# Performance work log

Hardware: AMD Instinct MI355X
Metric: run time of the kernel (lower is better)

The kernel has to match this reference:

```python
import jax, jax.numpy as jnp
import numpy as np

B, S, D = 4, 2048, 1024
H, DQ, DV = 16, 64, 64
LN_EPS = 1e-3  # keras LayerNormalization default


def _layer_norm(x, gamma, beta):
    mu = jnp.mean(x, axis=-1, keepdims=True)
    var = jnp.mean(jnp.square(x - mu), axis=-1, keepdims=True)
    return (x - mu) * jax.lax.rsqrt(var + LN_EPS) * gamma + beta


def setup_inputs() -> dict:
    key = jax.random.key(0)
    ks = jax.random.split(key, 6)
    x = jax.random.normal(ks[0], (B, S, D), jnp.float32)
    lengths = jax.random.randint(ks[1], (B,), 1, S + 1).astype(jnp.int32)
    scale = 0.02
    return {
        "query_sequences": x,
        "key_value_sequences": x,  # identical -> self-attention branch
        "key_value_sequence_lengths": lengths,
        "W_q": jax.random.normal(ks[2], (D, H * DQ), jnp.float32) * scale,
        "b_q": jnp.zeros((H * DQ,), jnp.float32),
        "W_kv": jax.random.normal(ks[3], (D, H * (DQ + DV)), jnp.float32) * scale,
        "b_kv": jnp.zeros((H * (DQ + DV),), jnp.float32),
        "W_o": jax.random.normal(ks[4], (H * DV, D), jnp.float32) * scale,
        "b_o": jnp.zeros((D,), jnp.float32),
        "ln_gamma": jnp.ones((D,), jnp.float32),
        "ln_beta": jnp.zeros((D,), jnp.float32),
    }


def reference(query_sequences, key_value_sequences, key_value_sequence_lengths,
              W_q, b_q, W_kv, b_kv, W_o, b_o, ln_gamma, ln_beta):
    # data-dependent self-attention detection, as in the TF code
    self_att = jnp.all(query_sequences == key_value_sequences)

    q_norm = _layer_norm(query_sequences, ln_gamma, ln_beta)
    kv_used = jnp.where(self_att, _layer_norm(key_value_sequences, ln_gamma, ln_beta),
                        key_value_sequences)
    residual = q_norm

    Q = (q_norm @ W_q + b_q).reshape(B, S, H, DQ)          # b q h d
    KV = kv_used @ W_kv + b_kv
    K = KV[..., : H * DQ].reshape(B, S, H, DQ)              # b k h d
    V = KV[..., H * DQ :].reshape(B, S, H, DV)              # b k h d

    scores = jnp.einsum("bqhd,bkhd->bhqk", Q, K) / np.sqrt(DQ).astype(np.float32)

    # key padding mask: key position < true length
    not_pad = (jnp.arange(S, dtype=jnp.int32)[None, None, None, :]
               < key_value_sequence_lengths[:, None, None, None])
    scores = jnp.where(not_pad, scores, -jnp.inf)
    # in_decoder=False -> no causal mask branch

    attn = jax.nn.softmax(scores, axis=-1)                  # dropout is identity at inference
    ctx = jnp.einsum("bhqk,bkhd->bqhd", attn, V).reshape(B, S, H * DV)
    out = ctx @ W_o + b_o + residual
    return out
```

## Files before the change

kernel.cpp:

```cpp
#include <hip/hip_runtime.h>
#include <hip/hip_bf16.h>
#include <cstdint>
#include <cmath>


#define DEV static __device__ __forceinline__

typedef float  f32x4 __attribute__((ext_vector_type(4)));
typedef short  s16x8 __attribute__((ext_vector_type(8)));
typedef short  s16x4 __attribute__((ext_vector_type(4)));
typedef __bf16 bf16x8 __attribute__((ext_vector_type(8)));
typedef unsigned int u32x4 __attribute__((ext_vector_type(4)));

DEV void gload_lds16(const void* g, void* l) {
  __builtin_amdgcn_global_load_lds(
      (const __attribute__((address_space(1))) unsigned int*)g,
      (__attribute__((address_space(3))) unsigned int*)l, 16, 0, 0);
}

DEV bf16x8 ldsv(const void* p) {
  return __builtin_bit_cast(bf16x8, *(const s16x8*)p);
}

DEV f32x4 mfma16(bf16x8 a, bf16x8 b, f32x4 c) {
  return __builtin_amdgcn_mfma_f32_16x16x32_bf16(a, b, c, 0, 0, 0);
}

DEV unsigned short f2b(float f) {
  __hip_bfloat16 h = __float2bfloat16(f);
  return __builtin_bit_cast(unsigned short, h);
}

DEV unsigned int cvt_pk_bf16(float lo, float hi) {
  unsigned int r;
  asm("v_cvt_pk_bf16_f32 %0, %1, %2" : "=v"(r) : "v"(lo), "v"(hi));
  return r;
}

__global__ __launch_bounds__(256) void ln_kernel(
    const float* __restrict__ x, const float* __restrict__ gamma,
    const float* __restrict__ beta, __hip_bfloat16* __restrict__ out)
{
  const int row = blockIdx.x, t = threadIdx.x;
  const float4 v = ((const float4*)(x + (size_t)row * 1024))[t];
  float s = v.x + v.y + v.z + v.w;
  float q = v.x * v.x + v.y * v.y + v.z * v.z + v.w * v.w;
#pragma unroll
  for (int m = 1; m < 64; m <<= 1) { s += __shfl_xor(s, m, 64); q += __shfl_xor(q, m, 64); }
  __shared__ float red[8];
  if ((t & 63) == 0) { red[t >> 6] = s; red[4 + (t >> 6)] = q; }
  __syncthreads();
  s = red[0] + red[1] + red[2] + red[3];
  q = red[4] + red[5] + red[6] + red[7];
  const float mu = s * (1.f / 1024.f);
  const float var = q * (1.f / 1024.f) - mu * mu;
  const float rs = rsqrtf(var + 1e-3f);
  const float4 g = ((const float4*)gamma)[t];
  const float4 bt = ((const float4*)beta)[t];
  s16x4 o;
  o[0] = (short)f2b((v.x - mu) * rs * g.x + bt.x);
  o[1] = (short)f2b((v.y - mu) * rs * g.y + bt.y);
  o[2] = (short)f2b((v.z - mu) * rs * g.z + bt.z);
  o[3] = (short)f2b((v.w - mu) * rs * g.w + bt.w);
  *(s16x4*)((short*)out + (size_t)row * 1024 + t * 4) = o;
}

__global__ __launch_bounds__(256) void wconv(
    const float* __restrict__ W, int N, __hip_bfloat16* __restrict__ Wt)
{
  __shared__ float tile[64][65];
  const int t = threadIdx.x;
  const int k0 = blockIdx.x * 64, n0 = blockIdx.y * 64;
#pragma unroll
  for (int p = 0; p < 4; ++p) {
    int r = p * 16 + (t >> 4), c4 = (t & 15) * 4;
    float4 v = *(const float4*)(W + (size_t)(k0 + r) * N + n0 + c4);
    tile[r][c4] = v.x; tile[r][c4 + 1] = v.y; tile[r][c4 + 2] = v.z; tile[r][c4 + 3] = v.w;
  }
  __syncthreads();
#pragma unroll
  for (int p = 0; p < 4; ++p) {
    int n = p * 16 + (t >> 4), kc = (t & 15) * 4;
    s16x4 o;
    o[0] = (short)f2b(tile[kc][n]);     o[1] = (short)f2b(tile[kc + 1][n]);
    o[2] = (short)f2b(tile[kc + 2][n]); o[3] = (short)f2b(tile[kc + 3][n]);
    *(s16x4*)((short*)Wt + (size_t)(n0 + n) * 1024 + k0 + kc) = o;
  }
}

template<bool RESID>
__global__ __launch_bounds__(256, 2) void gemm_bt(
    const __hip_bfloat16* __restrict__ A, const __hip_bfloat16* __restrict__ Bt,
    const float* __restrict__ bias0, const float* __restrict__ bias1, int split,
    const __hip_bfloat16* __restrict__ resid,
    __hip_bfloat16* __restrict__ outb, float* __restrict__ outf, int Ncols)
{
  __shared__ __align__(16) short sA[128 * 64];
  __shared__ __align__(16) short sB[128 * 64];
  const int t = threadIdx.x, l = t & 63, w = t >> 6;
  const int wr = w >> 1, wc = w & 1, lr = l & 15, lg = l >> 4;
  const int row0 = blockIdx.y * 128, col0 = blockIdx.x * 128;
  f32x4 acc[4][4] = {};

  for (int kt = 0; kt < 1024; kt += 64) {
#pragma unroll
    for (int p = 0; p < 4; ++p) {
      const int L = p * 4096 + t * 16;
      const int r = L >> 7, c = ((L >> 4) & 7) ^ (r & 7);
      gload_lds16((const char*)A + ((size_t)(row0 + r) * 1024 + kt + c * 8) * 2, (char*)sA + L);
    }
#pragma unroll
    for (int p = 0; p < 4; ++p) {
      const int L = p * 4096 + t * 16;
      const int r = L >> 7, c = ((L >> 4) & 7) ^ (r & 7);
      gload_lds16((const char*)Bt + ((size_t)(col0 + r) * 1024 + kt + c * 8) * 2, (char*)sB + L);
    }
    __syncthreads();

    bf16x8 af[4][2], bfr[4][2];
#pragma unroll
    for (int mb = 0; mb < 4; ++mb) {
      const int ar = wr * 64 + mb * 16 + lr;
#pragma unroll
      for (int kk = 0; kk < 2; ++kk)
        af[mb][kk] = ldsv((const char*)sA + ar * 128 + (((kk * 4 + lg) ^ (ar & 7)) * 16));
    }
#pragma unroll
    for (int nb = 0; nb < 4; ++nb) {
      const int br = wc * 64 + nb * 16 + lr;
#pragma unroll
      for (int kk = 0; kk < 2; ++kk)
        bfr[nb][kk] = ldsv((const char*)sB + br * 128 + (((kk * 4 + lg) ^ (br & 7)) * 16));
    }
#pragma unroll
    for (int kk = 0; kk < 2; ++kk)
#pragma unroll
      for (int mb = 0; mb < 4; ++mb)
#pragma unroll
        for (int nb = 0; nb < 4; ++nb)
          acc[mb][nb] = mfma16(af[mb][kk], bfr[nb][kk], acc[mb][nb]);
    __syncthreads();
  }

#pragma unroll
  for (int mb = 0; mb < 4; ++mb) {
    const int rbase = row0 + wr * 64 + mb * 16 + lg * 4;
#pragma unroll
    for (int nb = 0; nb < 4; ++nb) {
      const int col = col0 + wc * 64 + nb * 16 + lr;
      const float bias = (col < split) ? bias0[col] : bias1[col - split];
#pragma unroll
      for (int jr = 0; jr < 4; ++jr) {
        const size_t idx = (size_t)(rbase + jr) * Ncols + col;
        float v = acc[mb][nb][jr] + bias;
        if (RESID) outf[idx] = v + __bfloat162float(resid[idx]);
        else       outb[idx] = __float2bfloat16(v);
      }
    }
  }
}

__global__ __launch_bounds__(256) void vtrans(
    const __hip_bfloat16* __restrict__ qkv, __hip_bfloat16* __restrict__ vt)
{
  __shared__ __align__(16) short tile[64][72];
  const int t = threadIdx.x;
  const int s0 = blockIdx.x * 64;
  const int bh = blockIdx.y, b = bh >> 4, h = bh & 15;
#pragma unroll
  for (int p = 0; p < 2; ++p) {
    int idx = p * 256 + t;
    int r = idx >> 3, c = idx & 7;
    s16x8 vv = *(const s16x8*)((const short*)qkv +
        (size_t)(b * 2048 + s0 + r) * 3072 + 2048 + h * 64 + c * 8);
    *(s16x8*)((char*)tile + r * 144 + c * 16) = vv;
  }
  __syncthreads();
  const int dv = t >> 2, sc = (t & 3) * 16;
  s16x8 a, bvec;
#pragma unroll
  for (int e = 0; e < 8; ++e) a[e] = tile[sc + e][dv];
#pragma unroll
  for (int e = 0; e < 8; ++e) bvec[e] = tile[sc + 8 + e][dv];
  short* dst = (short*)vt + (size_t)(bh * 64 + dv) * 2048 + s0 + sc;
  *(s16x8*)dst = a;
  *(s16x8*)(dst + 8) = bvec;
}

__global__ __launch_bounds__(256, 4) void attn_kernel(
    const __hip_bfloat16* __restrict__ qkv, const __hip_bfloat16* __restrict__ vt,
    const int* __restrict__ lens, __hip_bfloat16* __restrict__ ctx)
{
  __shared__ __align__(16) short sK[2][64 * 64];
  __shared__ __align__(16) short sV[2][64 * 64];
  const int t = threadIdx.x, l = t & 63, w = t >> 6;
  const int lr = l & 15, lg = l >> 4;
  const int bh = blockIdx.y, b = bh >> 4, h = bh & 15;
  const int q0 = blockIdx.x * 128 + w * 32;
  const int len = lens[b];
  const float NEG = -__builtin_inff();
  const float QSC = 0.18033688f;

  bf16x8 qf[2][2];
#pragma unroll
  for (int mbt = 0; mbt < 2; ++mbt)
#pragma unroll
    for (int kk = 0; kk < 2; ++kk) {
      bf16x8 r = ldsv((const char*)qkv +
          ((size_t)(b * 2048 + q0 + mbt * 16 + lr) * 3072 + h * 64 + kk * 32 + lg * 8) * 2);
#pragma unroll
      for (int e = 0; e < 8; ++e) qf[mbt][kk][e] = (__bf16)((float)r[e] * QSC);
    }

  f32x4 o[4][2] = {};
  float mrun[2] = {NEG, NEG}, ssum[2] = {0.f, 0.f};

  auto stage = [&](short* dK, short* dV, int kv0) {
#pragma unroll
    for (int p = 0; p < 2; ++p) {
      const int L = p * 4096 + t * 16;
      const int r = L >> 7, c = ((L >> 4) & 7) ^ (r & 7);
      gload_lds16((const char*)qkv +
          ((size_t)(b * 2048 + kv0 + r) * 3072 + 1024 + h * 64 + c * 8) * 2, (char*)dK + L);
    }
#pragma unroll
    for (int p = 0; p < 2; ++p) {
      const int L = p * 4096 + t * 16;
      const int r = L >> 7, c = ((L >> 4) & 7) ^ (r & 7);
      gload_lds16((const char*)vt +
          ((size_t)(bh * 64 + r) * 2048 + kv0 + c * 8) * 2, (char*)dV + L);
    }
  };

  const int nt = (len + 63) >> 6;
  short* curK = sK[0]; short* nxtK = sK[1];
  short* curV = sV[0]; short* nxtV = sV[1];
  stage(curK, curV, 0);

  const int srcA = (lg & 1) * 32 + lr;
  const int srcB = srcA + 16;

  for (int ti = 0; ti < nt; ++ti) {
    const int kv0 = ti * 64;
    if (ti + 1 < nt) {
      stage(nxtK, nxtV, kv0 + 64);
      asm volatile("s_waitcnt vmcnt(4)" ::: "memory");
    } else {
      asm volatile("s_waitcnt vmcnt(0)" ::: "memory");
    }
    __builtin_amdgcn_s_barrier();
    asm volatile("" ::: "memory");

    f32x4 sf[2][4] = {};
    __builtin_amdgcn_s_setprio(1);
#pragma unroll
    for (int kk = 0; kk < 2; ++kk) {
      bf16x8 ak[4];
#pragma unroll
      for (int nbt = 0; nbt < 4; ++nbt) {
        const int br = nbt * 16 + lr;
        ak[nbt] = ldsv((const char*)curK + br * 128 + (((kk * 4 + lg) ^ (br & 7)) * 16));
      }
#pragma unroll
      for (int mbt = 0; mbt < 2; ++mbt)
#pragma unroll
        for (int nbt = 0; nbt < 4; ++nbt)
          sf[mbt][nbt] = mfma16(ak[nbt], qf[mbt][kk], sf[mbt][nbt]);
    }
    __builtin_amdgcn_s_setprio(0);

    if (kv0 + 64 > len) {
#pragma unroll
      for (int nbt = 0; nbt < 4; ++nbt)
#pragma unroll
        for (int jr = 0; jr < 4; ++jr)
          if (kv0 + nbt * 16 + lg * 4 + jr >= len) {
            sf[0][nbt][jr] = NEG;
            sf[1][nbt][jr] = NEG;
          }
    }

    float rm[2];
#pragma unroll
    for (int mbt = 0; mbt < 2; ++mbt) {
      f32x4 m4 = sf[mbt][0];
      m4 = __builtin_elementwise_max(m4, sf[mbt][1]);
      m4 = __builtin_elementwise_max(m4, sf[mbt][2]);
      m4 = __builtin_elementwise_max(m4, sf[mbt][3]);
      float m0 = fmaxf(fmaxf(m4[0], m4[1]), fmaxf(m4[2], m4[3]));
      m0 = fmaxf(m0, __shfl_xor(m0, 16, 64));
      m0 = fmaxf(m0, __shfl_xor(m0, 32, 64));
      rm[mbt] = m0;
    }
    const bool need = (rm[0] > mrun[0] + 3.f) || (rm[1] > mrun[1] + 3.f);
    if (__any(need)) {
#pragma unroll
      for (int mbt = 0; mbt < 2; ++mbt) {
        const float mnew = fmaxf(mrun[mbt], rm[mbt]);
        const float corr = __builtin_amdgcn_exp2f(mrun[mbt] - mnew);
        mrun[mbt] = mnew;
        ssum[mbt] *= corr;
#pragma unroll
        for (int nbt2 = 0; nbt2 < 4; ++nbt2) o[nbt2][mbt] *= corr;
      }
    }
    unsigned int W0[2][4], W1[2][4];
#pragma unroll
    for (int mbt = 0; mbt < 2; ++mbt) {
      f32x4 ts = {0.f, 0.f, 0.f, 0.f};
#pragma unroll
      for (int nbt = 0; nbt < 4; ++nbt) {
        f32x4 pe;
#pragma unroll
        for (int jr = 0; jr < 4; ++jr)
          pe[jr] = __builtin_amdgcn_exp2f(sf[mbt][nbt][jr] - mrun[mbt]);
        ts += pe;
        W0[mbt][nbt] = cvt_pk_bf16(pe[0], pe[1]);
        W1[mbt][nbt] = cvt_pk_bf16(pe[2], pe[3]);
      }
      ssum[mbt] += (ts[0] + ts[1]) + (ts[2] + ts[3]);
    }

#pragma unroll
    for (int c = 0; c < 2; ++c) {
      bf16x8 vf[4], pb[2];
#pragma unroll
      for (int nbt2 = 0; nbt2 < 4; ++nbt2) {
        const int vr = nbt2 * 16 + lr;
        vf[nbt2] = ldsv((const char*)curV + vr * 128 + (((c * 4 + lg) ^ (vr & 7)) * 16));
      }
#pragma unroll
      for (int mbt = 0; mbt < 2; ++mbt) {
        const unsigned int selW0 = (lg & 2) ? W0[mbt][2 * c + 1] : W0[mbt][2 * c];
        const unsigned int selW1 = (lg & 2) ? W1[mbt][2 * c + 1] : W1[mbt][2 * c];
        u32x4 bw;
        bw[0] = __shfl((int)selW0, srcA, 64);
        bw[1] = __shfl((int)selW1, srcA, 64);
        bw[2] = __shfl((int)selW0, srcB, 64);
        bw[3] = __shfl((int)selW1, srcB, 64);
        pb[mbt] = __builtin_bit_cast(bf16x8, bw);
      }
      __builtin_amdgcn_s_setprio(1);
#pragma unroll
      for (int nbt2 = 0; nbt2 < 4; ++nbt2)
#pragma unroll
        for (int mbt = 0; mbt < 2; ++mbt)
          o[nbt2][mbt] = mfma16(vf[nbt2], pb[mbt], o[nbt2][mbt]);
      __builtin_amdgcn_s_setprio(0);
    }

    asm volatile("s_waitcnt lgkmcnt(0)" ::: "memory");
    __builtin_amdgcn_s_barrier();
    asm volatile("" ::: "memory");
    short* tk = curK; curK = nxtK; nxtK = tk;
    short* tv = curV; curV = nxtV; nxtV = tv;
  }

  float inv[2];
#pragma unroll
  for (int mbt = 0; mbt < 2; ++mbt) {
    float s = ssum[mbt];
    s += __shfl_xor(s, 16, 64);
    s += __shfl_xor(s, 32, 64);
    inv[mbt] = 1.f / s;
  }
  char* eb = (char*)sK + w * 4352;
#pragma unroll
  for (int mbt = 0; mbt < 2; ++mbt)
#pragma unroll
    for (int nbt2 = 0; nbt2 < 4; ++nbt2)
#pragma unroll
      for (int jr = 0; jr < 4; ++jr)
        *(short*)(eb + (mbt * 16 + lr) * 136 + (nbt2 * 16 + lg * 4 + jr) * 2) =
            (short)f2b(o[nbt2][mbt][jr] * inv[mbt]);
  asm volatile("s_waitcnt lgkmcnt(0)" ::: "memory");
  __builtin_amdgcn_sched_barrier(0);
  const int qi = l >> 1, half = l & 1;
#pragma unroll
  for (int i = 0; i < 4; ++i) {
    s16x8 v = *(const s16x8*)(eb + qi * 136 + half * 64 + i * 16);
    *(s16x8*)((short*)ctx + (size_t)(b * 2048 + q0 + qi) * 1024 + h * 64 + half * 32 + i * 8) = v;
  }
}

extern "C" void kernel_launch(void* const* d_in, const int* in_sizes, int n_in,
                              void* d_out, int out_size, void* d_ws, size_t ws_size,
                              hipStream_t stream)
{
  const float* x     = (const float*)d_in[0];
  const int*   lens  = (const int*)d_in[2];
  const float* Wq    = (const float*)d_in[3];
  const float* bq    = (const float*)d_in[4];
  const float* Wkv   = (const float*)d_in[5];
  const float* bkv   = (const float*)d_in[6];
  const float* Wo    = (const float*)d_in[7];
  const float* bo    = (const float*)d_in[8];
  const float* gamma = (const float*)d_in[9];
  const float* beta  = (const float*)d_in[10];
  float* out = (float*)d_out;

  char* ws = (char*)d_ws;
  __hip_bfloat16* ln  = (__hip_bfloat16*)(ws);
  __hip_bfloat16* qkv = (__hip_bfloat16*)(ws + ((size_t)16 << 20));
  __hip_bfloat16* vt  = (__hip_bfloat16*)(ws + ((size_t)64 << 20));
  __hip_bfloat16* ctx = (__hip_bfloat16*)(ws + ((size_t)80 << 20));
  __hip_bfloat16* wt  = (__hip_bfloat16*)(ws + ((size_t)96 << 20));
  __hip_bfloat16* wot = (__hip_bfloat16*)(ws + ((size_t)102 << 20));

  ln_kernel<<<dim3(8192), dim3(256), 0, stream>>>(x, gamma, beta, ln);
  wconv<<<dim3(16, 16), dim3(256), 0, stream>>>(Wq, 1024, wt);
  wconv<<<dim3(16, 32), dim3(256), 0, stream>>>(Wkv, 2048, wt + (size_t)1024 * 1024);
  wconv<<<dim3(16, 16), dim3(256), 0, stream>>>(Wo, 1024, wot);
  gemm_bt<false><<<dim3(24, 64), dim3(256), 0, stream>>>(
      ln, wt, bq, bkv, 1024, (const __hip_bfloat16*)nullptr,
      qkv, (float*)nullptr, 3072);
  vtrans<<<dim3(32, 64), dim3(256), 0, stream>>>(qkv, vt);
  attn_kernel<<<dim3(16, 64), dim3(256), 0, stream>>>(qkv, vt, lens, ctx);
  gemm_bt<true><<<dim3(8, 64), dim3(256), 0, stream>>>(
      ctx, wot, bo, bo, 1 << 30, ln,
      (__hip_bfloat16*)nullptr, out, 1024);
}
```

Measured before the change: 174.9 us.

## Add 256x256 triple-buffered QKV GEMM and restructure attention to 16-row waves

Replaces the QKV projection GEMM with a new 512-thread kernel that uses 256x256 tiles, a three-stage LDS ring fed by direct global-to-LDS loads, interleaved barriers and an XCD-aware block remap. The attention kernel now gives each wave 16 query rows instead of 32, doubling the grid, with a swizzled block order. It also reads V fragments straight from global memory instead of staging them in LDS. The output GEMM loses its template and split-bias logic. These changes aim to raise GEMM data reuse and attention occupancy, at the cost of more K reloads per query and uncoalesced global V reads.

```diff
diff --git a/kernel.cpp b/kernel.cpp
--- a/kernel.cpp
+++ b/kernel.cpp
@@ -36,6 +36,8 @@
   asm("v_cvt_pk_bf16_f32 %0, %1, %2" : "=v"(r) : "v"(lo), "v"(hi));
   return r;
 }
+
+#define MEMFENCE asm volatile("" ::: "memory")
 
 __global__ __launch_bounds__(256) void ln_kernel(
     const float* __restrict__ x, const float* __restrict__ gamma,
@@ -88,12 +90,113 @@
   }
 }
 
-template<bool RESID>
+__global__ __launch_bounds__(512, 2) void gemm8(
+    const __hip_bfloat16* __restrict__ A, const __hip_bfloat16* __restrict__ Bt,
+    const float* __restrict__ bias0, const float* __restrict__ bias1, int split,
+    __hip_bfloat16* __restrict__ outb)
+{
+  __shared__ __align__(16) short sA[3 * 8192];
+  __shared__ __align__(16) short sB[3 * 8192];
+  const int t = threadIdx.x, l = t & 63, w = t >> 6;
+  const int wr = w >> 2, wc = w & 3, lr = l & 15, lg = l >> 4;
+  int bid = blockIdx.x;
+  const int cpx = gridDim.x >> 3;
+  bid = (bid & 7) * cpx + (bid >> 3);
+  const int bx = bid % 12, by = bid / 12;
+  const int row0 = by * 256, col0 = bx * 256;
+
+  f32x4 acc[8][4] = {};
+  const int NT = 32;
+
+  auto stageA = [&](int buf, int kt) {
+#pragma unroll
+    for (int p = 0; p < 2; ++p) {
+      const int L = p * 8192 + t * 16;
+      const int r = L >> 6, c = (L >> 4) & 3;
+      const int j = c ^ (r & 3);
+      gload_lds16((const char*)A + ((size_t)(row0 + r) * 1024 + kt + j * 8) * 2,
+                  (char*)sA + buf * 16384 + L);
+    }
+  };
+  auto stageB = [&](int buf, int kt) {
+#pragma unroll
+    for (int p = 0; p < 2; ++p) {
+      const int L = p * 8192 + t * 16;
+      const int r = L >> 6, c = (L >> 4) & 3;
+      const int j = c ^ (r & 3);
+      gload_lds16((const char*)Bt + ((size_t)(col0 + r) * 1024 + kt + j * 8) * 2,
+                  (char*)sB + buf * 16384 + L);
+    }
+  };
+
+  stageA(0, 0);  stageB(0, 0);
+  stageA(1, 32); stageB(1, 32);
+  asm volatile("s_waitcnt vmcnt(4)" ::: "memory");
+  MEMFENCE; __builtin_amdgcn_s_barrier(); MEMFENCE;
+
+#pragma unroll 1
+  for (int ti = 0; ti < NT; ++ti) {
+    const int cur = ti % 3, nx2 = (ti + 2) % 3;
+    const char* bA = (const char*)sA + cur * 16384;
+    const char* bB = (const char*)sB + cur * 16384;
+    bf16x8 bfr[4], af[4];
+#pragma unroll
+    for (int nb = 0; nb < 4; ++nb) {
+      const int br = wc * 64 + nb * 16 + lr;
+      bfr[nb] = ldsv(bB + br * 64 + ((lg ^ (br & 3)) * 16));
+    }
+#pragma unroll
+    for (int mb = 0; mb < 4; ++mb) {
+      const int ar = wr * 128 + mb * 16 + lr;
+      af[mb] = ldsv(bA + ar * 64 + ((lg ^ (ar & 3)) * 16));
+    }
+    if (ti + 2 < NT) stageA(nx2, (ti + 2) * 32);
+    MEMFENCE; __builtin_amdgcn_s_barrier(); MEMFENCE;
+    __builtin_amdgcn_s_setprio(1);
+#pragma unroll
+    for (int mb = 0; mb < 4; ++mb)
+#pragma unroll
+      for (int nb = 0; nb < 4; ++nb)
+        acc[mb][nb] = mfma16(af[mb], bfr[nb], acc[mb][nb]);
+    __builtin_amdgcn_s_setprio(0);
+    MEMFENCE; __builtin_amdgcn_s_barrier(); MEMFENCE;
+#pragma unroll
+    for (int mb = 0; mb < 4; ++mb) {
+      const int ar = wr * 128 + 64 + mb * 16 + lr;
+      af[mb] = ldsv(bA + ar * 64 + ((lg ^ (ar & 3)) * 16));
+    }
+    if (ti + 2 < NT) stageB(nx2, (ti + 2) * 32);
+    MEMFENCE; __builtin_amdgcn_s_barrier(); MEMFENCE;
+    __builtin_amdgcn_s_setprio(1);
+#pragma unroll
+    for (int mb = 0; mb < 4; ++mb)
+#pragma unroll
+      for (int nb = 0; nb < 4; ++nb)
+        acc[mb + 4][nb] = mfma16(af[mb], bfr[nb], acc[mb + 4][nb]);
+    __builtin_amdgcn_s_setprio(0);
+    if (ti + 2 < NT) asm volatile("s_waitcnt vmcnt(4)" ::: "memory");
+    else             asm volatile("s_waitcnt vmcnt(0)" ::: "memory");
+    MEMFENCE; __builtin_amdgcn_s_barrier(); MEMFENCE;
+  }
+
+#pragma unroll
+  for (int mb = 0; mb < 8; ++mb) {
+    const int rbase = row0 + wr * 128 + mb * 16 + lg * 4;
+#pragma unroll
+    for (int nb = 0; nb < 4; ++nb) {
+      const int col = col0 + wc * 64 + nb * 16 + lr;
+      const float bias = (col < split) ? bias0[col] : bias1[col - split];
+#pragma unroll
+      for (int jr = 0; jr < 4; ++jr)
+        outb[(size_t)(rbase + jr) * 3072 + col] = __float2bfloat16(acc[mb][nb][jr] + bias);
+    }
+  }
+}
+
 __global__ __launch_bounds__(256, 2) void gemm_bt(
     const __hip_bfloat16* __restrict__ A, const __hip_bfloat16* __restrict__ Bt,
-    const float* __restrict__ bias0, const float* __restrict__ bias1, int split,
-    const __hip_bfloat16* __restrict__ resid,
-    __hip_bfloat16* __restrict__ outb, float* __restrict__ outf, int Ncols)
+    const float* __restrict__ bias0,
+    const __hip_bfloat16* __restrict__ resid, float* __restrict__ outf)
 {
   __shared__ __align__(16) short sA[128 * 64];
   __shared__ __align__(16) short sB[128 * 64];
@@ -148,13 +251,11 @@
 #pragma unroll
     for (int nb = 0; nb < 4; ++nb) {
       const int col = col0 + wc * 64 + nb * 16 + lr;
-      const float bias = (col < split) ? bias0[col] : bias1[col - split];
+      const float bias = bias0[col];
 #pragma unroll
       for (int jr = 0; jr < 4; ++jr) {
-        const size_t idx = (size_t)(rbase + jr) * Ncols + col;
-        float v = acc[mb][nb][jr] + bias;
-        if (RESID) outf[idx] = v + __bfloat162float(resid[idx]);
-        else       outb[idx] = __float2bfloat16(v);
+        const size_t idx = (size_t)(rbase + jr) * 1024 + col;
+        outf[idx] = acc[mb][nb][jr] + bias + __bfloat162float(resid[idx]);
       }
     }
   }
@@ -192,30 +293,29 @@
     const int* __restrict__ lens, __hip_bfloat16* __restrict__ ctx)
 {
   __shared__ __align__(16) short sK[2][64 * 64];
-  __shared__ __align__(16) short sV[2][64 * 64];
   const int t = threadIdx.x, l = t & 63, w = t >> 6;
   const int lr = l & 15, lg = l >> 4;
-  const int bh = blockIdx.y, b = bh >> 4, h = bh & 15;
-  const int q0 = blockIdx.x * 128 + w * 32;
+  int bid = blockIdx.x;
+  bid = (bid & 7) * 256 + (bid >> 3);
+  const int qb = bid & 31, bh = bid >> 5, b = bh >> 4, h = bh & 15;
+  const int q0w = qb * 64 + w * 16;
   const int len = lens[b];
   const float NEG = -__builtin_inff();
   const float QSC = 0.18033688f;
 
-  bf16x8 qf[2][2];
-#pragma unroll
-  for (int mbt = 0; mbt < 2; ++mbt)
-#pragma unroll
-    for (int kk = 0; kk < 2; ++kk) {
-      bf16x8 r = ldsv((const char*)qkv +
-          ((size_t)(b * 2048 + q0 + mbt * 16 + lr) * 3072 + h * 64 + kk * 32 + lg * 8) * 2);
-#pragma unroll
-      for (int e = 0; e < 8; ++e) qf[mbt][kk][e] = (__bf16)((float)r[e] * QSC);
-    }
-
-  f32x4 o[4][2] = {};
-  float mrun[2] = {NEG, NEG}, ssum[2] = {0.f, 0.f};
-
-  auto stage = [&](short* dK, short* dV, int kv0) {
+  bf16x8 qf[2];
+#pragma unroll
+  for (int kk = 0; kk < 2; ++kk) {
+    bf16x8 r = ldsv((const char*)qkv +
+        ((size_t)(b * 2048 + q0w + lr) * 3072 + h * 64 + kk * 32 + lg * 8) * 2);
+#pragma unroll
+    for (int e = 0; e < 8; ++e) qf[kk][e] = (__bf16)((float)r[e] * QSC);
+  }
+
+  f32x4 o[4] = {};
+  float mrun = NEG, ssum = 0.f;
+
+  auto stageK = [&](short* dK, int kv0) {
 #pragma unroll
     for (int p = 0; p < 2; ++p) {
       const int L = p * 4096 + t * 16;
@@ -223,19 +323,11 @@
       gload_lds16((const char*)qkv +
           ((size_t)(b * 2048 + kv0 + r) * 3072 + 1024 + h * 64 + c * 8) * 2, (char*)dK + L);
     }
-#pragma unroll
-    for (int p = 0; p < 2; ++p) {
-      const int L = p * 4096 + t * 16;
-      const int r = L >> 7, c = ((L >> 4) & 7) ^ (r & 7);
-      gload_lds16((const char*)vt +
-          ((size_t)(bh * 64 + r) * 2048 + kv0 + c * 8) * 2, (char*)dV + L);
-    }
   };
 
   const int nt = (len + 63) >> 6;
   short* curK = sK[0]; short* nxtK = sK[1];
-  short* curV = sV[0]; short* nxtV = sV[1];
-  stage(curK, curV, 0);
+  stageK(curK, 0);
 
   const int srcA = (lg & 1) * 32 + lr;
   const int srcB = srcA + 16;
@@ -243,15 +335,22 @@
   for (int ti = 0; ti < nt; ++ti) {
     const int kv0 = ti * 64;
     if (ti + 1 < nt) {
-      stage(nxtK, nxtV, kv0 + 64);
-      asm volatile("s_waitcnt vmcnt(4)" ::: "memory");
+      stageK(nxtK, kv0 + 64);
+      asm volatile("s_waitcnt vmcnt(2)" ::: "memory");
     } else {
       asm volatile("s_waitcnt vmcnt(0)" ::: "memory");
     }
-    __builtin_amdgcn_s_barrier();
-    asm volatile("" ::: "memory");
-
-    f32x4 sf[2][4] = {};
+    MEMFENCE; __builtin_amdgcn_s_barrier(); MEMFENCE;
+
+    bf16x8 vf[4][2];
+#pragma unroll
+    for (int nbt2 = 0; nbt2 < 4; ++nbt2)
+#pragma unroll
+      for (int c = 0; c < 2; ++c)
+        vf[nbt2][c] = ldsv((const char*)vt +
+            ((size_t)(bh * 64 + nbt2 * 16 + lr) * 2048 + kv0 + (c * 4 + lg) * 8) * 2);
+
+    f32x4 sf[4] = {};
     __builtin_amdgcn_s_setprio(1);
 #pragma unroll
     for (int kk = 0; kk < 2; ++kk) {
@@ -262,10 +361,8 @@
         ak[nbt] = ldsv((const char*)curK + br * 128 + (((kk * 4 + lg) ^ (br & 7)) * 16));
       }
 #pragma unroll
-      for (int mbt = 0; mbt < 2; ++mbt)
-#pragma unroll
-        for (int nbt = 0; nbt < 4; ++nbt)
-          sf[mbt][nbt] = mfma16(ak[nbt], qf[mbt][kk], sf[mbt][nbt]);
+      for (int nbt = 0; nbt < 4; ++nbt)
+        sf[nbt] = mfma16(ak[nbt], qf[kk], sf[nbt]);
     }
     __builtin_amdgcn_s_setprio(0);
 
@@ -274,112 +371,81 @@
       for (int nbt = 0; nbt < 4; ++nbt)
 #pragma unroll
         for (int jr = 0; jr < 4; ++jr)
-          if (kv0 + nbt * 16 + lg * 4 + jr >= len) {
-            sf[0][nbt][jr] = NEG;
-            sf[1][nbt][jr] = NEG;
-          }
-    }
-
-    float rm[2];
-#pragma unroll
-    for (int mbt = 0; mbt < 2; ++mbt) {
-      f32x4 m4 = sf[mbt][0];
-      m4 = __builtin_elementwise_max(m4, sf[mbt][1]);
-      m4 = __builtin_elementwise_max(m4, sf[mbt][2]);
-      m4 = __builtin_elementwise_max(m4, sf[mbt][3]);
-      float m0 = fmaxf(fmaxf(m4[0], m4[1]), fmaxf(m4[2], m4[3]));
-      m0 = fmaxf(m0, __shfl_xor(m0, 16, 64));
-      m0 = fmaxf(m0, __shfl_xor(m0, 32, 64));
-      rm[mbt] = m0;
-    }
-    const bool need = (rm[0] > mrun[0] + 3.f) || (rm[1] > mrun[1] + 3.f);
-    if (__any(need)) {
-#pragma unroll
-      for (int mbt = 0; mbt < 2; ++mbt) {
-        const float mnew = fmaxf(mrun[mbt], rm[mbt]);
-        const float corr = __builtin_amdgcn_exp2f(mrun[mbt] - mnew);
-        mrun[mbt] = mnew;
-        ssum[mbt] *= corr;
-#pragma unroll
-        for (int nbt2 = 0; nbt2 < 4; ++nbt2) o[nbt2][mbt] *= corr;
-      }
-    }
-    unsigned int W0[2][4], W1[2][4];
-#pragma unroll
-    for (int mbt = 0; mbt < 2; ++mbt) {
+          if (kv0 + nbt * 16 + lg * 4 + jr >= len) sf[nbt][jr] = NEG;
+    }
+
+    f32x4 m4 = sf[0];
+    m4 = __builtin_elementwise_max(m4, sf[1]);
+    m4 = __builtin_elementwise_max(m4, sf[2]);
+    m4 = __builtin_elementwise_max(m4, sf[3]);
+    float rm = fmaxf(fmaxf(m4[0], m4[1]), fmaxf(m4[2], m4[3]));
+    rm = fmaxf(rm, __shfl_xor(rm, 16, 64));
+    rm = fmaxf(rm, __shfl_xor(rm, 32, 64));
+    if (__any(rm > mrun + 3.f)) {
+      const float mnew = fmaxf(mrun, rm);
+      const float corr = __builtin_amdgcn_exp2f(mrun - mnew);
+      mrun = mnew;
+      ssum *= corr;
+#pragma unroll
+      for (int nbt2 = 0; nbt2 < 4; ++nbt2) o[nbt2] *= corr;
+    }
+    unsigned int W0[4], W1[4];
+    {
       f32x4 ts = {0.f, 0.f, 0.f, 0.f};
 #pragma unroll
       for (int nbt = 0; nbt < 4; ++nbt) {
         f32x4 pe;
 #pragma unroll
         for (int jr = 0; jr < 4; ++jr)
-          pe[jr] = __builtin_amdgcn_exp2f(sf[mbt][nbt][jr] - mrun[mbt]);
+          pe[jr] = __builtin_amdgcn_exp2f(sf[nbt][jr] - mrun);
         ts += pe;
-        W0[mbt][nbt] = cvt_pk_bf16(pe[0], pe[1]);
-        W1[mbt][nbt] = cvt_pk_bf16(pe[2], pe[3]);
+        W0[nbt] = cvt_pk_bf16(pe[0], pe[1]);
+        W1[nbt] = cvt_pk_bf16(pe[2], pe[3]);
       }
-      ssum[mbt] += (ts[0] + ts[1]) + (ts[2] + ts[3]);
+      ssum += (ts[0] + ts[1]) + (ts[2] + ts[3]);
     }
 
 #pragma unroll
     for (int c = 0; c < 2; ++c) {
-      bf16x8 vf[4], pb[2];
-#pragma unroll
-      for (int nbt2 = 0; nbt2 < 4; ++nbt2) {
-        const int vr = nbt2 * 16 + lr;
-        vf[nbt2] = ldsv((const char*)curV + vr * 128 + (((c * 4 + lg) ^ (vr & 7)) * 16));
-      }
-#pragma unroll
-      for (int mbt = 0; mbt < 2; ++mbt) {
-        const unsigned int selW0 = (lg & 2) ? W0[mbt][2 * c + 1] : W0[mbt][2 * c];
-        const unsigned int selW1 = (lg & 2) ? W1[mbt][2 * c + 1] : W1[mbt][2 * c];
-        u32x4 bw;
-        bw[0] = __shfl((int)selW0, srcA, 64);
-        bw[1] = __shfl((int)selW1, srcA, 64);
-        bw[2] = __shfl((int)selW0, srcB, 64);
-        bw[3] = __shfl((int)selW1, srcB, 64);
-        pb[mbt] = __builtin_bit_cast(bf16x8, bw);
-      }
+      const unsigned int selW0 = (lg & 2) ? W0[2 * c + 1] : W0[2 * c];
+      const unsigned int selW1 = (lg & 2) ? W1[2 * c + 1] : W1[2 * c];
+      u32x4 bw;
+      bw[0] = __shfl((int)selW0, srcA, 64);
+      bw[1] = __shfl((int)selW1, srcA, 64);
+      bw[2] = __shfl((int)selW0, srcB, 64);
+      bw[3] = __shfl((int)selW1, srcB, 64);
+      const bf16x8 pb = __builtin_bit_cast(bf16x8, bw);
       __builtin_amdgcn_s_setprio(1);
 #pragma unroll
       for (int nbt2 = 0; nbt2 < 4; ++nbt2)
-#pragma unroll
-        for (int mbt = 0; mbt < 2; ++mbt)
-          o[nbt2][mbt] = mfma16(vf[nbt2], pb[mbt], o[nbt2][mbt]);
+        o[nbt2] = mfma16(vf[nbt2][c], pb, o[nbt2]);
       __builtin_amdgcn_s_setprio(0);
     }
 
     asm volatile("s_waitcnt lgkmcnt(0)" ::: "memory");
-    __builtin_amdgcn_s_barrier();
-    asm volatile("" ::: "memory");
+    MEMFENCE; __builtin_amdgcn_s_barrier(); MEMFENCE;
     short* tk = curK; curK = nxtK; nxtK = tk;
-    short* tv = curV; curV = nxtV; nxtV = tv;
-  }
-
-  float inv[2];
-#pragma unroll
-  for (int mbt = 0; mbt < 2; ++mbt) {
-    float s = ssum[mbt];
-    s += __shfl_xor(s, 16, 64);
-    s += __shfl_xor(s, 32, 64);
-    inv[mbt] = 1.f / s;
-  }
-  char* eb = (char*)sK + w * 4352;
-#pragma unroll
-  for (int mbt = 0; mbt < 2; ++mbt)
-#pragma unroll
-    for (int nbt2 = 0; nbt2 < 4; ++nbt2)
-#pragma unroll
-      for (int jr = 0; jr < 4; ++jr)
-        *(short*)(eb + (mbt * 16 + lr) * 136 + (nbt2 * 16 + lg * 4 + jr) * 2) =
-            (short)f2b(o[nbt2][mbt][jr] * inv[mbt]);
+  }
+
+  float s = ssum;
+  s += __shfl_xor(s, 16, 64);
+  s += __shfl_xor(s, 32, 64);
+  const float inv = 1.f / s;
+  char* eb = (char*)sK + w * 2176;
+#pragma unroll
+  for (int nbt2 = 0; nbt2 < 4; ++nbt2)
+#pragma unroll
+    for (int jr = 0; jr < 4; ++jr)
+      *(short*)(eb + lr * 136 + (nbt2 * 16 + lg * 4 + jr) * 2) =
+          (short)f2b(o[nbt2][jr] * inv);
   asm volatile("s_waitcnt lgkmcnt(0)" ::: "memory");
   __builtin_amdgcn_sched_barrier(0);
-  const int qi = l >> 1, half = l & 1;
-#pragma unroll
-  for (int i = 0; i < 4; ++i) {
-    s16x8 v = *(const s16x8*)(eb + qi * 136 + half * 64 + i * 16);
-    *(s16x8*)((short*)ctx + (size_t)(b * 2048 + q0 + qi) * 1024 + h * 64 + half * 32 + i * 8) = v;
+  const int qi = l >> 2, pt = l & 3;
+#pragma unroll
+  for (int i = 0; i < 2; ++i) {
+    const int ch = pt * 2 + i;
+    s16x8 v = *(const s16x8*)(eb + qi * 136 + ch * 16);
+    *(s16x8*)((short*)ctx + (size_t)(b * 2048 + q0w + qi) * 1024 + h * 64 + ch * 8) = v;
   }
 }
 
@@ -411,12 +477,8 @@
   wconv<<<dim3(16, 16), dim3(256), 0, stream>>>(Wq, 1024, wt);
   wconv<<<dim3(16, 32), dim3(256), 0, stream>>>(Wkv, 2048, wt + (size_t)1024 * 1024);
   wconv<<<dim3(16, 16), dim3(256), 0, stream>>>(Wo, 1024, wot);
-  gemm_bt<false><<<dim3(24, 64), dim3(256), 0, stream>>>(
-      ln, wt, bq, bkv, 1024, (const __hip_bfloat16*)nullptr,
-      qkv, (float*)nullptr, 3072);
+  gemm8<<<dim3(384), dim3(512), 0, stream>>>(ln, wt, bq, bkv, 1024, qkv);
   vtrans<<<dim3(32, 64), dim3(256), 0, stream>>>(qkv, vt);
-  attn_kernel<<<dim3(16, 64), dim3(256), 0, stream>>>(qkv, vt, lens, ctx);
-  gemm_bt<true><<<dim3(8, 64), dim3(256), 0, stream>>>(
-      ctx, wot, bo, bo, 1 << 30, ln,
-      (__hip_bfloat16*)nullptr, out, 1024);
-}
+  attn_kernel<<<dim3(2048), dim3(256), 0, stream>>>(qkv, vt, lens, ctx);
+  gemm_bt<<<dim3(8, 64), dim3(256), 0, stream>>>(ctx, wot, bo, ln, out);
+}
```

New measurement: 351.1 us. 2.01x slower.
